# Kernel tuning notes

Hardware: AMD Instinct MI355X
Metric: run time of the kernel (lower is better)

## Reference

```python
import jax, jax.numpy as jnp
import numpy as np

ROTARY_DIM = 32
THETA = 10000.0

def _rotate_half(t):
    # interleaved pairs: (..., d) -> rotate each (x1, x2) pair to (-x2, x1)
    x = t.reshape(t.shape[:-1] + (-1, 2))
    x1, x2 = x[..., 0], x[..., 1]
    return jnp.stack([-x2, x1], axis=-1).reshape(t.shape)

def _apply_rope(t, offset=0):
    # t: (B, h, T, dh); rotate only the first ROTARY_DIM dims
    T = t.shape[-2]
    inv_freq = 1.0 / (THETA ** (jnp.arange(0, ROTARY_DIM, 2, dtype=jnp.float32) / ROTARY_DIM))
    pos = jnp.arange(T, dtype=jnp.float32) + offset
    freqs = pos[:, None] * inv_freq[None, :]                 # (T, ROTARY_DIM/2)
    freqs = jnp.repeat(freqs, 2, axis=-1)                    # (T, ROTARY_DIM) interleaved
    cos, sin = jnp.cos(freqs), jnp.sin(freqs)
    t_rot, t_pass = t[..., :ROTARY_DIM], t[..., ROTARY_DIM:]
    t_rot = t_rot * cos + _rotate_half(t_rot) * sin
    return jnp.concatenate([t_rot, t_pass], axis=-1)

def setup_inputs() -> dict:
    key = jax.random.key(0)
    k1, k2, k3 = jax.random.split(key, 3)
    B, T, dim = 4, 1024, 1024
    x = jax.random.normal(k1, (B, T, dim), dtype=jnp.float32)
    Wqkv = jax.random.normal(k2, (dim, 3 * dim), dtype=jnp.float32) * (dim ** -0.5)
    Wout = jax.random.normal(k3, (dim, dim), dtype=jnp.float32) * (dim ** -0.5)
    return {"x": x, "Wqkv": Wqkv, "Wout": Wout}

def reference(x, Wqkv, Wout):
    B, T, dim = x.shape
    n_heads = 16
    dh = dim // n_heads
    qkv = x @ Wqkv                                            # (B, T, 3*dim)
    qkv = qkv.reshape(B, T, 3, n_heads, dh)
    qkv = jnp.transpose(qkv, (2, 0, 3, 1, 4))                 # (3, B, h, T, dh)
    q, k, v = qkv[0], qkv[1], qkv[2]
    q = _apply_rope(q, offset=0)
    k = _apply_rope(k, offset=0)
    scale = 1.0 / jnp.sqrt(jnp.asarray(dh, dtype=x.dtype))
    scores = jnp.einsum('bhqd,bhkd->bhqk', q, k) * scale      # (B, h, T, T)
    causal = jnp.tril(jnp.ones((T, T), dtype=bool))
    scores = jnp.where(causal, scores, jnp.asarray(-jnp.inf, dtype=scores.dtype))
    attn = jax.nn.softmax(scores, axis=-1)
    out = jnp.einsum('bhqk,bhkd->bhqd', attn, v)              # (B, h, T, dh)
    out = jnp.transpose(out, (0, 2, 1, 3)).reshape(B, T, dim)
    return out @ Wout
```

## Files before the change

kernel.cpp:

```cpp
#include <hip/hip_runtime.h>
#include <cstdint>
#include <cstddef>

typedef __bf16 bf16;
typedef __bf16 bf16x8 __attribute__((ext_vector_type(8)));
typedef float f32x4 __attribute__((ext_vector_type(4)));

#define DEVINL __device__ __forceinline__

static constexpr int Tn   = 1024;
static constexpr int DIM  = 1024;
static constexpr int NH   = 16;
static constexpr int DH   = 64;
static constexpr int QKVN = 3072;

DEVINL void g2l16(const void* g, void* l) {
  __builtin_amdgcn_global_load_lds(
      (const __attribute__((address_space(1))) void*)g,
      (__attribute__((address_space(3))) void*)l, 16, 0, 0);
}


__global__ void k_f32_to_bf16(const float* __restrict__ in, bf16* __restrict__ out, int n4) {
  int i = blockIdx.x * blockDim.x + threadIdx.x;
  if (i >= n4) return;
  float4 v = reinterpret_cast<const float4*>(in)[i];
  bf16 o[4] = {(bf16)v.x, (bf16)v.y, (bf16)v.z, (bf16)v.w};
  reinterpret_cast<uint2*>(out)[i] = *reinterpret_cast<uint2*>(o);
}

__global__ void k_transpose_w(const float* __restrict__ in, bf16* __restrict__ out, int K, int N) {
  __shared__ float tile[32][33];
  int n0 = blockIdx.x * 32, k0 = blockIdx.y * 32;
  int tx = threadIdx.x, ty = threadIdx.y;
#pragma unroll
  for (int j = 0; j < 32; j += 8)
    tile[ty + j][tx] = in[(size_t)(k0 + ty + j) * N + n0 + tx];
  __syncthreads();
#pragma unroll
  for (int j = 0; j < 32; j += 8)
    out[(size_t)(n0 + ty + j) * K + k0 + tx] = (bf16)tile[tx][ty + j];
}

__global__ void k_rope(bf16* __restrict__ qkv) {
  int idx = blockIdx.x * 256 + threadIdx.x;
  int i = idx & 15;
  int h = (idx >> 4) & 15;
  int w = (idx >> 8) & 1;
  int t = (idx >> 9) & 1023;
  int b = idx >> 19;
  float inv = exp2f(-(float)(2 * i) * (13.287712379549449f / 32.0f));
  float ang = (float)t * inv;
  float sn, cs;
  sincosf(ang, &sn, &cs);
  size_t base = ((size_t)(b * Tn + t)) * QKVN + (size_t)w * DIM + h * DH + 2 * i;
  float x1 = (float)qkv[base], x2 = (float)qkv[base + 1];
  qkv[base]     = (bf16)(x1 * cs - x2 * sn);
  qkv[base + 1] = (bf16)(x2 * cs + x1 * sn);
}

__global__ void k_transpose_v(const bf16* __restrict__ qkv, bf16* __restrict__ vt) {
  __shared__ bf16 tile[32][33];
  int t0 = blockIdx.x * 32, d0 = blockIdx.y * 32;
  int bh = blockIdx.z;
  int b = bh >> 4, h = bh & 15;
  int tx = threadIdx.x, ty = threadIdx.y;
#pragma unroll
  for (int j = 0; j < 32; j += 8)
    tile[ty + j][tx] = qkv[((size_t)(b * Tn + t0 + ty + j)) * QKVN + 2 * DIM + h * DH + d0 + tx];
  __syncthreads();
#pragma unroll
  for (int j = 0; j < 32; j += 8)
    vt[((size_t)(bh * DH + d0 + ty + j)) * Tn + t0 + tx] = tile[tx][ty + j];
}

template <bool F32OUT>
__global__ __launch_bounds__(256) void k_gemm_bt(
    const bf16* __restrict__ A, const bf16* __restrict__ Bt,
    void* __restrict__ Cp, int M, int N, int K) {
  __shared__ bf16 As[128 * 64];
  __shared__ bf16 Bs[128 * 64];
  const int tid  = threadIdx.x;
  const int wave = tid >> 6, lane = tid & 63;
  const int lrow = lane & 15, quad = lane >> 4;
  const int m0 = blockIdx.y * 128, n0 = blockIdx.x * 128;
  const int wm = (wave >> 1) * 64, wn = (wave & 1) * 64;

  f32x4 acc[4][4];
#pragma unroll
  for (int mi = 0; mi < 4; mi++)
#pragma unroll
    for (int ni = 0; ni < 4; ni++) acc[mi][ni] = 0.f;

  for (int k0 = 0; k0 < K; k0 += 64) {
    __syncthreads();
#pragma unroll
    for (int i = 0; i < 4; i++) {
      int li = i * 256 + tid;
      int row = li >> 3, c = li & 7;
      int gc = c ^ (row & 7);
      g2l16(A + (size_t)(m0 + row) * K + k0 + gc * 8, As + li * 8);
    }
#pragma unroll
    for (int i = 0; i < 4; i++) {
      int li = i * 256 + tid;
      int row = li >> 3, c = li & 7;
      int gc = c ^ (row & 7);
      g2l16(Bt + (size_t)(n0 + row) * K + k0 + gc * 8, Bs + li * 8);
    }
    __syncthreads();
#pragma unroll
    for (int ki = 0; ki < 2; ki++) {
      bf16x8 af[4], bfr[4];
#pragma unroll
      for (int mi = 0; mi < 4; mi++) {
        int r = wm + mi * 16 + lrow;
        int pc = (ki * 4 + quad) ^ (r & 7);
        af[mi] = *reinterpret_cast<const bf16x8*>(As + r * 64 + pc * 8);
      }
#pragma unroll
      for (int ni = 0; ni < 4; ni++) {
        int r = wn + ni * 16 + lrow;
        int pc = (ki * 4 + quad) ^ (r & 7);
        bfr[ni] = *reinterpret_cast<const bf16x8*>(Bs + r * 64 + pc * 8);
      }
#pragma unroll
      for (int mi = 0; mi < 4; mi++)
#pragma unroll
        for (int ni = 0; ni < 4; ni++)
          acc[mi][ni] = __builtin_amdgcn_mfma_f32_16x16x32_bf16(af[mi], bfr[ni], acc[mi][ni], 0, 0, 0);
    }
  }

#pragma unroll
  for (int mi = 0; mi < 4; mi++)
#pragma unroll
    for (int ni = 0; ni < 4; ni++) {
      int col = n0 + wn + ni * 16 + lrow;
#pragma unroll
      for (int r = 0; r < 4; r++) {
        int row = m0 + wm + mi * 16 + quad * 4 + r;
        float v = acc[mi][ni][r];
        if (F32OUT)
          reinterpret_cast<float*>(Cp)[(size_t)row * N + col] = v;
        else
          reinterpret_cast<bf16*>(Cp)[(size_t)row * N + col] = (bf16)v;
      }
    }
}

__global__ __launch_bounds__(256) void k_attn(
    const bf16* __restrict__ qkv, const bf16* __restrict__ vt,
    bf16* __restrict__ ao) {
  __shared__ bf16 Ks[2][64 * 64];
  __shared__ bf16 Vs[2][64 * 64];
  __shared__ bf16 Ps[4][16 * 64];

  const int tid  = threadIdx.x;
  const int wave = tid >> 6, lane = tid & 63;
  const int lrow = lane & 15, quad = lane >> 4;
  const int bh = blockIdx.y, b = bh >> 4, h = bh & 15;
  const int q0 = blockIdx.x * 64;
  const int qw = q0 + wave * 16;
  const size_t qbase = (size_t)b * Tn * QKVN;

  bf16x8 qf[2];
  {
    const bf16* qp = qkv + qbase + (size_t)(qw + lrow) * QKVN + h * DH;
    qf[0] = *reinterpret_cast<const bf16x8*>(qp + quad * 8);
    qf[1] = *reinterpret_cast<const bf16x8*>(qp + 32 + quad * 8);
    const float SC = 0.125f * 1.44269504088896f;
#pragma unroll
    for (int j = 0; j < 8; j++) {
      qf[0][j] = (bf16)((float)qf[0][j] * SC);
      qf[1][j] = (bf16)((float)qf[1][j] * SC);
    }
  }

  f32x4 oa[4];
#pragma unroll
  for (int g = 0; g < 4; g++) oa[g] = 0.f;
  float li[4] = {0.f, 0.f, 0.f, 0.f};

  const int ktiles = blockIdx.x + 1;

  auto stage = [&](int k0, int bufi) {
#pragma unroll
    for (int i = 0; i < 2; i++) {
      int li2 = i * 256 + tid;
      int row = li2 >> 3, c = li2 & 7;
      int gc = c ^ (row & 7);
      g2l16(qkv + qbase + (size_t)(k0 + row) * QKVN + DIM + h * DH + gc * 8,
            &Ks[bufi][li2 * 8]);
      g2l16(vt + ((size_t)bh * DH + row) * Tn + k0 + gc * 8,
            &Vs[bufi][li2 * 8]);
    }
  };

  stage(0, 0);

  for (int kt = 0; kt < ktiles; kt++) {
    const int buf = kt & 1;
    __syncthreads();
    if (kt + 1 < ktiles) stage((kt + 1) << 6, buf ^ 1);

    const bf16* ks = Ks[buf];
    const bf16* vs = Vs[buf];

    f32x4 s[4];
#pragma unroll
    for (int g = 0; g < 4; g++) s[g] = 0.f;
#pragma unroll
    for (int kh = 0; kh < 2; kh++) {
      const int cX = ((kh * 4 + quad) ^ (lrow & 7)) << 3;
#pragma unroll
      for (int g = 0; g < 4; g++) {
        bf16x8 kf = *reinterpret_cast<const bf16x8*>(ks + (g * 16 + lrow) * 64 + cX);
        s[g] = __builtin_amdgcn_mfma_f32_16x16x32_bf16(qf[kh], kf, s[g], 0, 0, 0);
      }
    }

    const bool lastt = (kt == ktiles - 1);
#pragma unroll
    for (int g = 0; g < 4; g++) {
#pragma unroll
      for (int r = 0; r < 4; r++) {
        float p = exp2f(s[g][r]);
        if (lastt) {
          int kglob = (kt << 6) + g * 16 + lrow;
          int qi = qw + quad * 4 + r;
          p = (kglob <= qi) ? p : 0.f;
        }
        li[r] += p;
        int m = quad * 4 + r;
        int chunk = g * 2 + (lrow >> 3);
        Ps[wave][m * 64 + ((chunk ^ (m & 7)) << 3) + (lrow & 7)] = (bf16)p;
      }
    }

#pragma unroll
    for (int kh = 0; kh < 2; kh++) {
      const int cX = ((kh * 4 + quad) ^ (lrow & 7)) << 3;
      bf16x8 pf = *reinterpret_cast<const bf16x8*>(Ps[wave] + lrow * 64 + cX);
#pragma unroll
      for (int g = 0; g < 4; g++) {
        bf16x8 vf = *reinterpret_cast<const bf16x8*>(vs + (g * 16 + lrow) * 64 + cX);
        oa[g] = __builtin_amdgcn_mfma_f32_16x16x32_bf16(pf, vf, oa[g], 0, 0, 0);
      }
    }
  }

#pragma unroll
  for (int r = 0; r < 4; r++) {
    li[r] += __shfl_xor(li[r], 1, 64);
    li[r] += __shfl_xor(li[r], 2, 64);
    li[r] += __shfl_xor(li[r], 4, 64);
    li[r] += __shfl_xor(li[r], 8, 64);
  }

#pragma unroll
  for (int r = 0; r < 4; r++) {
    float inv = 1.0f / li[r];
    int row = qw + quad * 4 + r;
    bf16* dst = ao + ((size_t)b * Tn + row) * DIM + h * DH;
    dst[ 0 + lrow] = (bf16)(oa[0][r] * inv);
    dst[16 + lrow] = (bf16)(oa[1][r] * inv);
    dst[32 + lrow] = (bf16)(oa[2][r] * inv);
    dst[48 + lrow] = (bf16)(oa[3][r] * inv);
  }
}

extern "C" void kernel_launch(void* const* d_in, const int* in_sizes, int n_in,
                              void* d_out, int out_size, void* d_ws, size_t ws_size,
                              hipStream_t stream) {
  const float* x    = (const float*)d_in[0];
  const float* Wqkv = (const float*)d_in[1];
  const float* Wout = (const float*)d_in[2];
  char* ws = (char*)d_ws;

  bf16* xb    = (bf16*)(ws + 0);
  bf16* wqkvT = (bf16*)(ws + 8388608);
  bf16* woutT = (bf16*)(ws + 14680064);
  bf16* qkv   = (bf16*)(ws + 16777216);
  bf16* vt    = (bf16*)(ws + 41943040);
  bf16* ao    = (bf16*)(ws + 50331648);

  k_f32_to_bf16<<<4096, 256, 0, stream>>>(x, xb, 1048576);
  k_transpose_w<<<dim3(96, 32), dim3(32, 8), 0, stream>>>(Wqkv, wqkvT, 1024, 3072);
  k_transpose_w<<<dim3(32, 32), dim3(32, 8), 0, stream>>>(Wout, woutT, 1024, 1024);
  k_gemm_bt<false><<<dim3(24, 32), 256, 0, stream>>>(xb, wqkvT, (void*)qkv, 4096, 3072, 1024);
  k_rope<<<8192, 256, 0, stream>>>(qkv);
  k_transpose_v<<<dim3(32, 2, 64), dim3(32, 8), 0, stream>>>(qkv, vt);
  k_attn<<<dim3(16, 64), 256, 0, stream>>>(qkv, vt, ao);
  k_gemm_bt<true><<<dim3(8, 32), 256, 0, stream>>>(ao, woutT, d_out, 4096, 1024, 1024);
  (void)in_sizes; (void)n_in; (void)out_size; (void)ws_size;
}
```

Measured before the change: 194.3 us.

## Pair near and far query tiles per attention block to balance causal work

Each attention block now handles two query tiles, jn and 15-jn, sharing the staged K/V tiles, so every block does the same amount of causal work and the grid is halved. K/V loads are reused across both tiles. The QK MFMA operands are swapped so each lane holds a column of scores, which lets P be written to LDS as packed 4-wide vectors and the row sum be reduced with fewer shuffles. The cost is more registers per thread and a larger P buffer in LDS, which may lower occupancy.

Result: faster. 176.2 us (-9.3%).

```diff
diff --git a/kernel.cpp b/kernel.cpp
--- a/kernel.cpp
+++ b/kernel.cpp
@@ -3,6 +3,7 @@
 #include <cstddef>
 
 typedef __bf16 bf16;
+typedef __bf16 bf16x4 __attribute__((ext_vector_type(4)));
 typedef __bf16 bf16x8 __attribute__((ext_vector_type(8)));
 typedef float f32x4 __attribute__((ext_vector_type(4)));
 
@@ -154,35 +155,42 @@
     bf16* __restrict__ ao) {
   __shared__ bf16 Ks[2][64 * 64];
   __shared__ bf16 Vs[2][64 * 64];
-  __shared__ bf16 Ps[4][16 * 64];
+  __shared__ bf16 Ps[8][16 * 64];
 
   const int tid  = threadIdx.x;
   const int wave = tid >> 6, lane = tid & 63;
   const int lrow = lane & 15, quad = lane >> 4;
   const int bh = blockIdx.y, b = bh >> 4, h = bh & 15;
-  const int q0 = blockIdx.x * 64;
-  const int qw = q0 + wave * 16;
+  const int jn = blockIdx.x;
+  const int jf = 15 - jn;
+  const int qwf = jf * 64 + wave * 16;
+  const int qwn = jn * 64 + wave * 16;
   const size_t qbase = (size_t)b * Tn * QKVN;
 
-  bf16x8 qf[2];
+  bf16x8 qff[2], qfn[2];
   {
-    const bf16* qp = qkv + qbase + (size_t)(qw + lrow) * QKVN + h * DH;
-    qf[0] = *reinterpret_cast<const bf16x8*>(qp + quad * 8);
-    qf[1] = *reinterpret_cast<const bf16x8*>(qp + 32 + quad * 8);
     const float SC = 0.125f * 1.44269504088896f;
+    const bf16* qpf = qkv + qbase + (size_t)(qwf + lrow) * QKVN + h * DH;
+    const bf16* qpn = qkv + qbase + (size_t)(qwn + lrow) * QKVN + h * DH;
+    qff[0] = *reinterpret_cast<const bf16x8*>(qpf + quad * 8);
+    qff[1] = *reinterpret_cast<const bf16x8*>(qpf + 32 + quad * 8);
+    qfn[0] = *reinterpret_cast<const bf16x8*>(qpn + quad * 8);
+    qfn[1] = *reinterpret_cast<const bf16x8*>(qpn + 32 + quad * 8);
 #pragma unroll
     for (int j = 0; j < 8; j++) {
-      qf[0][j] = (bf16)((float)qf[0][j] * SC);
-      qf[1][j] = (bf16)((float)qf[1][j] * SC);
+      qff[0][j] = (bf16)((float)qff[0][j] * SC);
+      qff[1][j] = (bf16)((float)qff[1][j] * SC);
+      qfn[0][j] = (bf16)((float)qfn[0][j] * SC);
+      qfn[1][j] = (bf16)((float)qfn[1][j] * SC);
     }
   }
 
-  f32x4 oa[4];
-#pragma unroll
-  for (int g = 0; g < 4; g++) oa[g] = 0.f;
-  float li[4] = {0.f, 0.f, 0.f, 0.f};
-
-  const int ktiles = blockIdx.x + 1;
+  f32x4 oaf[4], oan[4];
+#pragma unroll
+  for (int g = 0; g < 4; g++) { oaf[g] = 0.f; oan[g] = 0.f; }
+  float lif = 0.f, lin = 0.f;
+
+  const int ntiles = jf + 1;
 
   auto stage = [&](int k0, int bufi) {
 #pragma unroll
@@ -197,16 +205,8 @@
     }
   };
 
-  stage(0, 0);
-
-  for (int kt = 0; kt < ktiles; kt++) {
-    const int buf = kt & 1;
-    __syncthreads();
-    if (kt + 1 < ktiles) stage((kt + 1) << 6, buf ^ 1);
-
-    const bf16* ks = Ks[buf];
-    const bf16* vs = Vs[buf];
-
+  auto unit = [&](const bf16* ks, const bf16* vs, bf16x8 (&qf)[2], f32x4 (&oa)[4],
+                  float& li, int pi, bool diag) {
     f32x4 s[4];
 #pragma unroll
     for (int g = 0; g < 4; g++) s[g] = 0.f;
@@ -216,57 +216,74 @@
 #pragma unroll
       for (int g = 0; g < 4; g++) {
         bf16x8 kf = *reinterpret_cast<const bf16x8*>(ks + (g * 16 + lrow) * 64 + cX);
-        s[g] = __builtin_amdgcn_mfma_f32_16x16x32_bf16(qf[kh], kf, s[g], 0, 0, 0);
-      }
-    }
-
-    const bool lastt = (kt == ktiles - 1);
+        s[g] = __builtin_amdgcn_mfma_f32_16x16x32_bf16(kf, qf[kh], s[g], 0, 0, 0);
+      }
+    }
+    float psum = 0.f;
+    const int qrel = wave * 16 + lrow;
 #pragma unroll
     for (int g = 0; g < 4; g++) {
+      bf16x4 pk;
 #pragma unroll
       for (int r = 0; r < 4; r++) {
         float p = exp2f(s[g][r]);
-        if (lastt) {
-          int kglob = (kt << 6) + g * 16 + lrow;
-          int qi = qw + quad * 4 + r;
-          p = (kglob <= qi) ? p : 0.f;
+        if (diag) {
+          int kl = g * 16 + quad * 4 + r;
+          p = (kl <= qrel) ? p : 0.f;
         }
-        li[r] += p;
-        int m = quad * 4 + r;
-        int chunk = g * 2 + (lrow >> 3);
-        Ps[wave][m * 64 + ((chunk ^ (m & 7)) << 3) + (lrow & 7)] = (bf16)p;
-      }
-    }
-
+        psum += p;
+        pk[r] = (bf16)p;
+      }
+      int chunk = 2 * g + (quad >> 1);
+      *reinterpret_cast<bf16x4*>(
+          Ps[pi] + lrow * 64 + ((chunk ^ (lrow & 7)) << 3) + 4 * (quad & 1)) = pk;
+    }
+    li += psum;
 #pragma unroll
     for (int kh = 0; kh < 2; kh++) {
       const int cX = ((kh * 4 + quad) ^ (lrow & 7)) << 3;
-      bf16x8 pf = *reinterpret_cast<const bf16x8*>(Ps[wave] + lrow * 64 + cX);
+      bf16x8 pf = *reinterpret_cast<const bf16x8*>(Ps[pi] + lrow * 64 + cX);
 #pragma unroll
       for (int g = 0; g < 4; g++) {
         bf16x8 vf = *reinterpret_cast<const bf16x8*>(vs + (g * 16 + lrow) * 64 + cX);
         oa[g] = __builtin_amdgcn_mfma_f32_16x16x32_bf16(pf, vf, oa[g], 0, 0, 0);
       }
     }
+  };
+
+  stage(0, 0);
+
+  for (int kt = 0; kt < ntiles; kt++) {
+    const int buf = kt & 1;
+    __syncthreads();
+    if (kt + 1 < ntiles) stage((kt + 1) << 6, buf ^ 1);
+
+    const bf16* ks = Ks[buf];
+    const bf16* vs = Vs[buf];
+
+    unit(ks, vs, qff, oaf, lif, wave * 2 + 0, kt == jf);
+    if (kt <= jn)
+      unit(ks, vs, qfn, oan, lin, wave * 2 + 1, kt == jn);
   }
 
+  lif += __shfl_xor(lif, 16, 64); lif += __shfl_xor(lif, 32, 64);
+  lin += __shfl_xor(lin, 16, 64); lin += __shfl_xor(lin, 32, 64);
+
 #pragma unroll
   for (int r = 0; r < 4; r++) {
-    li[r] += __shfl_xor(li[r], 1, 64);
-    li[r] += __shfl_xor(li[r], 2, 64);
-    li[r] += __shfl_xor(li[r], 4, 64);
-    li[r] += __shfl_xor(li[r], 8, 64);
-  }
-
-#pragma unroll
-  for (int r = 0; r < 4; r++) {
-    float inv = 1.0f / li[r];
-    int row = qw + quad * 4 + r;
-    bf16* dst = ao + ((size_t)b * Tn + row) * DIM + h * DH;
-    dst[ 0 + lrow] = (bf16)(oa[0][r] * inv);
-    dst[16 + lrow] = (bf16)(oa[1][r] * inv);
-    dst[32 + lrow] = (bf16)(oa[2][r] * inv);
-    dst[48 + lrow] = (bf16)(oa[3][r] * inv);
+    int m = quad * 4 + r;
+    float invf = 1.0f / __shfl(lif, m, 64);
+    float invn = 1.0f / __shfl(lin, m, 64);
+    bf16* dstf = ao + ((size_t)b * Tn + qwf + m) * DIM + h * DH;
+    bf16* dstn = ao + ((size_t)b * Tn + qwn + m) * DIM + h * DH;
+    dstf[ 0 + lrow] = (bf16)(oaf[0][r] * invf);
+    dstf[16 + lrow] = (bf16)(oaf[1][r] * invf);
+    dstf[32 + lrow] = (bf16)(oaf[2][r] * invf);
+    dstf[48 + lrow] = (bf16)(oaf[3][r] * invf);
+    dstn[ 0 + lrow] = (bf16)(oan[0][r] * invn);
+    dstn[16 + lrow] = (bf16)(oan[1][r] * invn);
+    dstn[32 + lrow] = (bf16)(oan[2][r] * invn);
+    dstn[48 + lrow] = (bf16)(oan[3][r] * invn);
   }
 }
 
@@ -291,7 +308,7 @@
   k_gemm_bt<false><<<dim3(24, 32), 256, 0, stream>>>(xb, wqkvT, (void*)qkv, 4096, 3072, 1024);
   k_rope<<<8192, 256, 0, stream>>>(qkv);
   k_transpose_v<<<dim3(32, 2, 64), dim3(32, 8), 0, stream>>>(qkv, vt);
-  k_attn<<<dim3(16, 64), 256, 0, stream>>>(qkv, vt, ao);
+  k_attn<<<dim3(8, 64), 256, 0, stream>>>(qkv, vt, ao);
   k_gemm_bt<true><<<dim3(8, 32), 256, 0, stream>>>(ao, woutT, d_out, 4096, 1024, 1024);
   (void)in_sizes; (void)n_in; (void)out_size; (void)ws_size;
 }
```
